# Performance work log

Hardware: AMD Instinct MI355X
Metric: run time of the kernel (lower is better)

Reference implementation:

```python
import jax, jax.numpy as jnp
import numpy as np


def _c1(x, W, b):
    # 1x1 conv: W [out,in], x [B,in,H,W]
    return jnp.einsum('oi,bihw->bohw', W, x) + b[None, :, None, None]


def _c3(x, W, b):
    # 3x3 conv, stride 1, padding 1 (SAME)
    y = jax.lax.conv_general_dilated(x, W, (1, 1), 'SAME',
                                     dimension_numbers=('NCHW', 'OIHW', 'NCHW'))
    return y + b[None, :, None, None]


def _resize(x, h, w):
    # matches torch F.interpolate(mode='bilinear', align_corners=False)
    return jax.image.resize(x, (x.shape[0], x.shape[1], h, w), 'linear', antialias=False)


def setup_inputs() -> dict:
    key = jax.random.key(0)
    ks = jax.random.split(key, 20)
    B, C, H, W = 4, 64, 128, 128
    d = C // 8

    def n(k, shape, s=0.05):
        return jax.random.normal(k, shape, dtype=jnp.float32) * s

    z = lambda c: jnp.zeros((c,), jnp.float32)
    return {
        'x': jax.random.normal(ks[0], (B, C, H, W), dtype=jnp.float32),
        'mask': jax.random.normal(ks[1], (B, 64, H, W), dtype=jnp.float32),
        'Wq': n(ks[2], (d, C)), 'bq': z(d),
        'Wk': n(ks[3], (d, C)), 'bk': z(d),
        'Wv': n(ks[4], (C, C)), 'bv': z(C),
        'alpha1': jax.random.uniform(ks[5], (1,), dtype=jnp.float32),
        'alpha2': jax.random.uniform(ks[6], (1,), dtype=jnp.float32),
        'mq_w1': n(ks[7], (64, 64, 3, 3)), 'mq_b1': z(64),
        'mq_w2': n(ks[8], (d, 64)), 'mq_b2': z(d),
        'mk_w1': n(ks[9], (64, 64, 3, 3)), 'mk_b1': z(64),
        'mk_w2': n(ks[10], (d, 64)), 'mk_b2': z(d),
        'ca_w1': n(ks[11], (64, 64)), 'ca_b1': z(64),
        'ca_w2': n(ks[12], (64, 64)), 'ca_b2': z(64),
    }


def reference(x, mask, Wq, bq, Wk, bk, Wv, bv, alpha1, alpha2,
              mq_w1, mq_b1, mq_w2, mq_b2, mk_w1, mk_b1, mk_w2, mk_b2,
              ca_w1, ca_b1, ca_w2, ca_b2):
    B, C, H, W = x.shape
    h2, w2 = H // 2, W // 2
    N = h2 * w2

    mask_q = _c1(jax.nn.relu(_c3(mask, mq_w1, mq_b1)), mq_w2, mq_b2)
    mask_k = _c1(jax.nn.relu(_c3(mask, mk_w1, mk_b1)), mk_w2, mk_b2)
    xq = _c1(x, Wq, bq)  # [B, d, H, W]
    xk = _c1(x, Wk, bk)

    pq = mask_q * xq * alpha1 + xq * (1.0 - alpha1)
    pq = _resize(pq, h2, w2).reshape(B, -1, N)          # [B, d, N]
    pk = mask_k * xk * alpha2 + xk * (1.0 - alpha2)
    pk = _resize(pk, h2, w2).reshape(B, -1, N)          # [B, d, N]

    energy = jnp.einsum('bdn,bdm->bnm', pq, pk)         # [B, N, N]
    attn = jax.nn.softmax(energy, axis=-1)

    pv = _resize(_c1(x, Wv, bv), h2, w2).reshape(B, C, N)
    out = jnp.einsum('bcn,bmn->bcm', pv, attn)          # value @ attn^T
    out = out.reshape(B, C, h2, w2)
    out = _resize(out, H, W)
    out = _c1(jax.nn.relu(_c1(out, ca_w1, ca_b1)), ca_w2, ca_b2)
    return out + x
```

## Files before the change

### kernel.cpp

```cpp
#include <hip/hip_runtime.h>
#include <hip/hip_bf16.h>

typedef _Float16 half8 __attribute__((ext_vector_type(8)));
typedef _Float16 half4v __attribute__((ext_vector_type(4)));
typedef _Float16 half2v __attribute__((ext_vector_type(2)));
typedef __fp16 pkh2 __attribute__((ext_vector_type(2)));
typedef float f32x4 __attribute__((ext_vector_type(4)));

static __device__ __forceinline__ f32x4 mfma16(half8 a, half8 b, f32x4 c) {
    return __builtin_amdgcn_mfma_f32_16x16x32_f16(a, b, c, 0, 0, 0);
}

typedef const __attribute__((address_space(1))) unsigned int* gas_ptr;
typedef __attribute__((address_space(3))) unsigned int* las_ptr;
static __device__ __forceinline__ void gload16(const void* g, void* l) {
    __builtin_amdgcn_global_load_lds((gas_ptr)g, (las_ptr)l, 16, 0, 0);
}

static __device__ __forceinline__ half2v cvt2(float a, float b) {
    pkh2 t = __builtin_amdgcn_cvt_pkrtz(a, b);
    return __builtin_bit_cast(half2v, t);
}
static __device__ __forceinline__ half8 pk8(f32x4 a, f32x4 b) {
    half2v x0 = cvt2(a[0], a[1]);
    half2v x1 = cvt2(a[2], a[3]);
    half2v x2 = cvt2(b[0], b[1]);
    half2v x3 = cvt2(b[2], b[3]);
    half4v lo = __builtin_shufflevector(x0, x1, 0, 1, 2, 3);
    half4v hi = __builtin_shufflevector(x2, x3, 0, 1, 2, 3);
    return __builtin_shufflevector(lo, hi, 0, 1, 2, 3, 4, 5, 6, 7);
}
static __device__ __forceinline__ half4v pk4(f32x4 a) {
    half2v x0 = cvt2(a[0], a[1]);
    half2v x1 = cvt2(a[2], a[3]);
    return __builtin_shufflevector(x0, x1, 0, 1, 2, 3);
}

#define WS_APCONV   0u
#define WS_APW2S    147456u
#define WS_APCA     151552u
#define WS_APW2K4   159744u
#define WS_PACKED   196608u
#define WS_MASKQ    8849408u
#define WS_MASKK    10946560u
#define WS_Q16      13043712u
#define WS_K16      13305856u
#define WS_V16      13568000u
#define WS_ZB       15665152u
#define WS_PACC8    17762304u
#define WS_PML8     34539520u
#define WS_END8     35063808u
#define WS_PACC4    WS_PACKED
#define WS_PML4     WS_MASKQ

__global__ __launch_bounds__(256) void prep_pack_kernel(
    const float* __restrict__ mask,
    const float* __restrict__ mqw1, const float* __restrict__ mkw1,
    const float* __restrict__ mqw2, const float* __restrict__ mkw2,
    const float* __restrict__ caw1, const float* __restrict__ caw2,
    _Float16* __restrict__ packed,
    _Float16* __restrict__ ApackConv, _Float16* __restrict__ ApackW2s,
    _Float16* __restrict__ ApackCA, _Float16* __restrict__ ApackW2K4)
{
    int tid = threadIdx.x;
    if (blockIdx.z < 4) {
        int ich = blockIdx.y, b = blockIdx.z;
        _Float16* Pb = packed + ((size_t)b * 8 + ich) * 130 * 130 * 8;
        if (blockIdx.x < 2) {
            for (int p = blockIdx.x * 260 + tid; p < (int)(blockIdx.x + 1) * 260; p += 256) {
                int row, col;
                if (p < 130)      { row = 0;       col = p; }
                else if (p < 260) { row = 129;     col = p - 130; }
                else if (p < 390) { row = p - 260; col = 0; }
                else              { row = p - 390; col = 129; }
                half8 z = {};
                *(half8*)(Pb + ((size_t)row * 130 + col) * 8) = z;
            }
        }
        int x = tid & 127;
        int sy = blockIdx.x * 2 + (tid >> 7);
        half8 v;
#pragma unroll
        for (int cc = 0; cc < 8; cc++)
            v[cc] = (_Float16)mask[(((size_t)(b * 64 + ich * 8 + cc)) * 128 + sy) * 128 + x];
        *(half8*)(Pb + (((size_t)(sy + 1)) * 130 + (x + 1)) * 8) = v;
        return;
    }
    int tid0 = (blockIdx.y * 64 + blockIdx.x) * 256 + tid;
    const int stride = 512 * 256;
    for (int idx = tid0; idx < 73728; idx += stride) {
        int j = idx & 7, lane = (idx >> 3) & 63, mf = (idx >> 9) & 3;
        int ks18 = idx >> 11;
        int br = ks18 / 18, kstep = ks18 % 18;
        int oc = mf * 16 + (lane & 15);
        int g = lane >> 4;
        int k = kstep * 32 + g * 8 + j;
        int tap = k >> 6, ic = k & 63;
        int dy = tap / 3, dx = tap - dy * 3;
        const float* w1 = br ? mkw1 : mqw1;
        ApackConv[idx] = (_Float16)w1[((oc * 64 + ic) * 3 + dy) * 3 + dx];
    }
    for (int idx = tid0; idx < 2048; idx += stride) {
        int j = idx & 7, lane = (idx >> 3) & 63;
        int f = (idx >> 9) & 1, br = idx >> 10;
        int dc = lane & 15, g = lane >> 4;
        int kap = 16 * (2 * f + (j >> 2)) + 4 * g + (j & 3);
        const float* w2 = br ? mkw2 : mqw2;
        ApackW2s[idx] = (_Float16)((dc < 8) ? w2[dc * 64 + kap] : 0.f);
    }
    for (int idx = tid0; idx < 4096; idx += stride) {
        int j = idx & 7, lane = (idx >> 3) & 63, mf = (idx >> 9) & 3, f = idx >> 11;
        int cp = mf * 16 + (lane & 15), g = lane >> 4;
        int kap = 16 * (2 * f + (j >> 2)) + 4 * g + (j & 3);
        ApackCA[idx] = (_Float16)caw1[cp * 64 + kap];
    }
    for (int idx = tid0; idx < 4096; idx += stride) {
        int j = idx & 7, lane = (idx >> 3) & 63, mf = (idx >> 9) & 3, f = idx >> 11;
        int cc = mf * 16 + (lane & 15), g = lane >> 4;
        int cpk = f * 32 + g * 8 + j;
        ApackW2K4[idx] = (_Float16)caw2[cc * 64 + cpk];
    }
}

__global__ __launch_bounds__(256) void conv_mask_kernel(
    const _Float16* __restrict__ packed,
    const _Float16* __restrict__ ApackConv,
    const _Float16* __restrict__ ApackW2s,
    const float* __restrict__ mqb1, const float* __restrict__ mqb2,
    const float* __restrict__ mkb1, const float* __restrict__ mkb2,
    _Float16* __restrict__ maskq, _Float16* __restrict__ maskk)
{
    __shared__ __align__(16) _Float16 A[36864];
    __shared__ __align__(16) _Float16 S[28032];
    int tid = threadIdx.x;
    int lane = tid & 63, w = tid >> 6;
    int x0 = blockIdx.x * 64;
    int y0 = blockIdx.y * 4;
    int bz = blockIdx.z;
    int b = bz >> 1, br = bz & 1;
    int q = lane & 15, g = lane >> 4;

    const _Float16* Ag = ApackConv + br * 36864;
#pragma unroll
    for (int i = 0; i < 18; i++) {
        int off = w * 9216 + i * 512;
        gload16(Ag + off + lane * 8, A + off);
    }
    const _Float16* Pb = packed + (size_t)b * 8 * 130 * 130 * 8;
#pragma unroll
    for (int i = 0; i < 12; i++) {
        int rr = w * 12 + i;
        int ich = rr / 6, pr = rr - ich * 6;
        const _Float16* src = Pb + (((size_t)ich * 130 + (y0 + pr)) * 130 + x0) * 8;
        _Float16* dst = S + (ich * 6 + pr) * 584;
        gload16(src + lane * 8, dst);
        if (lane < 8) gload16(src + (64 + lane) * 8, dst + 512);
    }
    __syncthreads();

    f32x4 acc[4][4] = {};
#pragma unroll
    for (int kstep = 0; kstep < 18; kstep++) {
        int tap = kstep >> 1;
        int dyv = tap / 3, dxv = tap - dyv * 3;
        int ich = (kstep & 1) * 4 + g;
        const _Float16* srow = S + ((ich * 6 + w + dyv) * 73 + q + dxv) * 8;
        half8 bf[4];
#pragma unroll
        for (int nf = 0; nf < 4; nf++)
            bf[nf] = *(const half8*)(srow + nf * 128);
        const _Float16* Ak = A + kstep * 2048 + lane * 8;
#pragma unroll
        for (int mf = 0; mf < 4; mf++) {
            half8 af = *(const half8*)(Ak + mf * 512);
#pragma unroll
            for (int nf = 0; nf < 4; nf++)
                acc[mf][nf] = mfma16(af, bf[nf], acc[mf][nf]);
        }
    }
    const float* b1p = br ? mkb1 : mqb1;
    const float* b2p = br ? mkb2 : mqb2;
    _Float16* outp = br ? maskk : maskq;
    float b1v[16];
#pragma unroll
    for (int mf = 0; mf < 4; mf++)
#pragma unroll
        for (int r = 0; r < 4; r++) b1v[mf * 4 + r] = b1p[mf * 16 + g * 4 + r];
    f32x4 acc2[4] = {};
#pragma unroll
    for (int f = 0; f < 2; f++) {
        half8 a2 = *(const half8*)(ApackW2s + (br * 2 + f) * 512 + lane * 8);
#pragma unroll
        for (int nf = 0; nf < 4; nf++) {
            half8 b2f;
#pragma unroll
            for (int j = 0; j < 8; j++) {
                int mfj = 2 * f + (j >> 2), rj = j & 3;
                b2f[j] = (_Float16)fmaxf(acc[mfj][nf][rj] + b1v[mfj * 4 + rj], 0.f);
            }
            acc2[nf] = mfma16(a2, b2f, acc2[nf]);
        }
    }
    if (g < 2) {
        int y = y0 + w;
#pragma unroll
        for (int r = 0; r < 4; r++) {
            int dc = g * 4 + r;
            float bb = b2p[dc];
#pragma unroll
            for (int nf = 0; nf < 4; nf++)
                outp[((size_t)(b * 8 + dc) * 128 + y) * 128 + (x0 + nf * 16 + q)] =
                    (_Float16)(acc2[nf][r] + bb);
        }
    }
}

__global__ __launch_bounds__(512) void proj_kernel(
    const float* __restrict__ xg,
    const _Float16* __restrict__ maskq, const _Float16* __restrict__ maskk,
    const float* __restrict__ Wq, const float* __restrict__ bq,
    const float* __restrict__ Wk, const float* __restrict__ bk,
    const float* __restrict__ Wv, const float* __restrict__ bv,
    const float* __restrict__ a1p, const float* __restrict__ a2p,
    _Float16* __restrict__ Qg, _Float16* __restrict__ Kg, _Float16* __restrict__ Vg)
{
    __shared__ float xr[16384];
    __shared__ float xw[4096];
    __shared__ float lWv[4096], lWq[512], lWk[512];
    int tid = threadIdx.x;
    int b = blockIdx.x >> 6, i = blockIdx.x & 63;

    for (int idx = tid; idx < 16384; idx += 512) {
        int ic = idx >> 8, rem = idx & 255;
        xr[idx] = xg[((size_t)(b * 64 + ic) * 128 + (2 * i + (rem >> 7))) * 128 + (rem & 127)];
    }
    for (int idx = tid; idx < 4096; idx += 512) lWv[idx] = Wv[idx];
    lWq[tid] = Wq[tid];
    lWk[tid] = Wk[tid];
    __syncthreads();
    for (int idx = tid; idx < 4096; idx += 512) {
        int ic = idx >> 6, j = idx & 63;
        const float* base = &xr[ic * 256 + 2 * j];
        xw[idx] = 0.25f * (base[0] + base[1] + base[128] + base[129]);
    }
    __syncthreads();

    if (tid < 256) {
        int c0 = tid >> 5;
        int j0 = (tid & 31) * 2;
        float acc0[8], acc1[8];
#pragma unroll
        for (int u = 0; u < 8; u++) { float bb = bv[c0 + 8 * u]; acc0[u] = bb; acc1[u] = bb; }
        for (int ic = 0; ic < 64; ic++) {
            float x0v = xw[ic * 64 + j0], x1v = xw[ic * 64 + j0 + 1];
#pragma unroll
            for (int u = 0; u < 8; u++) {
                float ww = lWv[(c0 + 8 * u) * 64 + ic];
                acc0[u] += ww * x0v; acc1[u] += ww * x1v;
            }
        }
        int f = j0 >> 5, gg = (j0 & 15) >> 2, hi = (j0 >> 4) & 1;
        int off = (f * 4 + gg) * 8 + (j0 & 3) + 4 * hi;
#pragma unroll
        for (int u = 0; u < 8; u++) {
            int c = c0 + 8 * u;
            _Float16* p = Vg + (size_t)(b * 64 + c) * 4096 + i * 64 + off;
            p[0] = (_Float16)acc0[u]; p[1] = (_Float16)acc1[u];
        }
    } else {
        int t = tid - 256;
        int branch = t >> 7;
        int ysel = t & 1;
        int j = (t >> 1) & 63;
        const float* W = branch ? lWk : lWq;
        const float* bias = branch ? bk : bq;
        float alpha = branch ? a2p[0] : a1p[0];
        const _Float16* mq = branch ? maskk : maskq;
        _Float16* outg = branch ? Kg : Qg;
        int x0c = 2 * j, x1c = 2 * j + 1;
        float aq0[8], aq1[8];
#pragma unroll
        for (int dc = 0; dc < 8; dc++) { float bb = bias[dc]; aq0[dc] = bb; aq1[dc] = bb; }
        for (int ic = 0; ic < 64; ic++) {
            float xv0 = xr[ic * 256 + ysel * 128 + x0c];
            float xv1 = xr[ic * 256 + ysel * 128 + x1c];
#pragma unroll
            for (int dc = 0; dc < 8; dc++) {
                float ww = W[dc * 64 + ic];
                aq0[dc] += ww * xv0; aq1[dc] += ww * xv1;
            }
        }
        int yy = 2 * i + ysel;
        half8 vq;
#pragma unroll
        for (int dc = 0; dc < 8; dc++) {
            size_t mbase = ((size_t)(b * 8 + dc) * 128 + yy) * 128;
            float m0v = (float)mq[mbase + x0c], m1v = (float)mq[mbase + x1c];
            float s = aq0[dc] * (alpha * m0v + (1.f - alpha))
                    + aq1[dc] * (alpha * m1v + (1.f - alpha));
            s += __shfl_xor(s, 1);
            vq[dc] = (_Float16)(0.25f * s);
        }
        if (ysel == 0)
            *(half8*)(outg + ((size_t)b * 4096 + i * 64 + j) * 8) = vq;
    }
}

__global__ __launch_bounds__(512, 4) void attn_kernel(
    const _Float16* __restrict__ Qg, const _Float16* __restrict__ Kg,
    const _Float16* __restrict__ Vg, const _Float16* __restrict__ ApackCA,
    _Float16* __restrict__ pacc, float* __restrict__ pml,
    int bmask, int sshift, int bbase)
{
    __shared__ __align__(16) _Float16 Vlds[8 * 4096];
    __shared__ __align__(16) _Float16 Klds[8 * 512];
    int tid = threadIdx.x, lane = tid & 63, w = tid >> 6;
    int q = lane & 15, g = lane >> 4;
    int bid = blockIdx.x;
    int qt = bid & 15, b = bbase + ((bid >> 4) & bmask), s = bid >> sshift;

    const _Float16* Kb = Kg + ((size_t)b * 4096 + s * 512) * 8;
    const _Float16* Vbase = Vg + (size_t)b * 64 * 4096 + s * 512;

    {
        gload16(Kb + (size_t)(w * 64 + lane) * 8, Klds + w * 512);
        int cc = w * 8 + (lane >> 3);
        int chl = (lane & 7) ^ (cc & 7);
        const _Float16* src0 = Vbase + (size_t)cc * 4096 + chl * 8;
#pragma unroll
        for (int t = 0; t < 8; t++)
            gload16(src0 + t * 64, Vlds + t * 4096 + w * 512);
    }
    half8 qf0 = {}, qf1 = {};
    if (g == 0) {
        int qb = qt * 256 + w * 32 + q;
        half8 r0 = *(const half8*)(Qg + ((size_t)b * 4096 + qb) * 8);
        half8 r1 = *(const half8*)(Qg + ((size_t)b * 4096 + qb + 16) * 8);
#pragma unroll
        for (int j = 0; j < 8; j++) {
            qf0[j] = (_Float16)((float)r0[j] * 1.44269504f);
            qf1[j] = (_Float16)((float)r1[j] * 1.44269504f);
        }
    }
    half8 a3[8];
#pragma unroll
    for (int i = 0; i < 8; i++) a3[i] = *(const half8*)(ApackCA + i * 512 + lane * 8);
    __syncthreads();

    half8 ones;
#pragma unroll
    for (int j = 0; j < 8; j++) ones[j] = (_Float16)1.f;

    f32x4 acc0[4] = {}, acc1[4] = {};
    f32x4 accl0 = {}, accl1 = {};
    const f32x4 zero4 = {};

#pragma unroll 2
    for (int t = 0; t < 8; t++) {
        const _Float16* Kt = Klds + t * 512;
        half8 af0 = *(const half8*)(Kt + q * 8);
        half8 af1 = *(const half8*)(Kt + (16 + q) * 8);
        half8 af2 = *(const half8*)(Kt + (32 + q) * 8);
        half8 af3 = *(const half8*)(Kt + (48 + q) * 8);

        half8 pb00, pb01, pb10, pb11;
        {
            f32x4 s0 = mfma16(af0, qf0, zero4);
            f32x4 s1 = mfma16(af1, qf0, zero4);
            f32x4 s2 = mfma16(af2, qf0, zero4);
            f32x4 s3 = mfma16(af3, qf0, zero4);
            f32x4 e0, e1, e2, e3;
#pragma unroll
            for (int r = 0; r < 4; r++) {
                e0[r] = __builtin_amdgcn_exp2f(s0[r]);
                e1[r] = __builtin_amdgcn_exp2f(s1[r]);
                e2[r] = __builtin_amdgcn_exp2f(s2[r]);
                e3[r] = __builtin_amdgcn_exp2f(s3[r]);
            }
            pb00 = pk8(e0, e1); pb01 = pk8(e2, e3);
            accl0 = mfma16(ones, pb00, accl0);
            accl0 = mfma16(ones, pb01, accl0);
        }
        {
            f32x4 s0 = mfma16(af0, qf1, zero4);
            f32x4 s1 = mfma16(af1, qf1, zero4);
            f32x4 s2 = mfma16(af2, qf1, zero4);
            f32x4 s3 = mfma16(af3, qf1, zero4);
            f32x4 e0, e1, e2, e3;
#pragma unroll
            for (int r = 0; r < 4; r++) {
                e0[r] = __builtin_amdgcn_exp2f(s0[r]);
                e1[r] = __builtin_amdgcn_exp2f(s1[r]);
                e2[r] = __builtin_amdgcn_exp2f(s2[r]);
                e3[r] = __builtin_amdgcn_exp2f(s3[r]);
            }
            pb10 = pk8(e0, e1); pb11 = pk8(e2, e3);
            accl1 = mfma16(ones, pb10, accl1);
            accl1 = mfma16(ones, pb11, accl1);
        }
        const _Float16* Vl = Vlds + t * 4096;
        int sw = q & 7;
        __builtin_amdgcn_s_setprio(1);
#pragma unroll
        for (int mfc = 0; mfc < 4; mfc++) {
            const _Float16* vr = Vl + (mfc * 16 + q) * 64;
            half8 av0 = *(const half8*)(vr + (g ^ sw) * 8);
            half8 av1 = *(const half8*)(vr + ((4 + g) ^ sw) * 8);
            acc0[mfc] = mfma16(av0, pb00, acc0[mfc]);
            acc1[mfc] = mfma16(av0, pb10, acc1[mfc]);
            acc0[mfc] = mfma16(av1, pb01, acc0[mfc]);
            acc1[mfc] = mfma16(av1, pb11, acc1[mfc]);
        }
        __builtin_amdgcn_s_setprio(0);
    }

    {
        half8 ob0 = pk8(acc0[0], acc0[1]);
        half8 ob1 = pk8(acc0[2], acc0[3]);
        f32x4 z[4] = {};
#pragma unroll
        for (int mf2 = 0; mf2 < 4; mf2++) {
            z[mf2] = mfma16(a3[mf2], ob0, z[mf2]);
            z[mf2] = mfma16(a3[4 + mf2], ob1, z[mf2]);
        }
        size_t prow = ((size_t)bid * 256 + w * 32 + q) * 64;
#pragma unroll
        for (int mf2 = 0; mf2 < 4; mf2++)
            *(half4v*)(pacc + prow + mf2 * 16 + g * 4) = pk4(z[mf2]);
        if (g == 0) pml[bid * 256 + w * 32 + q] = accl0[0];
    }
    {
        half8 ob0 = pk8(acc1[0], acc1[1]);
        half8 ob1 = pk8(acc1[2], acc1[3]);
        f32x4 z[4] = {};
#pragma unroll
        for (int mf2 = 0; mf2 < 4; mf2++) {
            z[mf2] = mfma16(a3[mf2], ob0, z[mf2]);
            z[mf2] = mfma16(a3[4 + mf2], ob1, z[mf2]);
        }
        size_t prow = ((size_t)bid * 256 + w * 32 + 16 + q) * 64;
#pragma unroll
        for (int mf2 = 0; mf2 < 4; mf2++)
            *(half4v*)(pacc + prow + mf2 * 16 + g * 4) = pk4(z[mf2]);
        if (g == 0) pml[bid * 256 + w * 32 + 16 + q] = accl1[0];
    }
}

__global__ __launch_bounds__(256) void combine_kernel(
    const _Float16* __restrict__ pacc, const float* __restrict__ pml,
    const float* __restrict__ cb1, _Float16* __restrict__ zb,
    int tps, int bbase)
{
    int T = blockIdx.x * 256 + threadIdx.x;
    int e = T & 7, row = T >> 3;
    int brel = row >> 12, qg = row & 4095;
    int qt16 = qg >> 8, ql = qg & 255;
    int tb0 = brel * 16 + qt16;

    float sum[8] = {};
    float L = 0.f;
    for (int s = 0; s < 8; s++) {
        int tile = s * tps + tb0;
        half8 v = *(const half8*)(pacc + ((size_t)tile * 256 + ql) * 64 + e * 8);
#pragma unroll
        for (int i = 0; i < 8; i++) sum[i] += (float)v[i];
        L += pml[tile * 256 + ql];
    }
    float inv = 1.f / L;
    half8 o;
#pragma unroll
    for (int i = 0; i < 8; i++) o[i] = (_Float16)(sum[i] * inv + cb1[e * 8 + i]);
    *(half8*)(zb + ((size_t)(bbase + brel) * 4096 + qg) * 64 + e * 8) = o;
}

template <int FUSED>
__global__ __launch_bounds__(512) void post_kernel(
    const _Float16* __restrict__ zg,
    const _Float16* __restrict__ pacc, const float* __restrict__ pml,
    const float* __restrict__ cb1,
    const float* __restrict__ xg,
    const _Float16* __restrict__ ApackW2K4, const float* __restrict__ cb2,
    float* __restrict__ outg)
{
    __shared__ _Float16 zt[6 * 18 * 72];
    int tid = threadIdx.x, lane = tid & 63, w = tid >> 6;
    int x0 = blockIdx.x * 32, y0 = blockIdx.y * 8, b = blockIdx.z;
    int r0 = 4 * (int)blockIdx.y - 1;
    int cbs = 16 * (int)blockIdx.x - 1;
    const _Float16* zgb = zg + (size_t)b * 4096 * 64;
    for (int idx = tid; idx < 864; idx += 512) {
        int rowi = idx >> 3, ch = idx & 7;
        int r = rowi / 18, col = rowi - r * 18;
        int zr = min(max(r0 + r, 0), 63);
        int zc = min(max(cbs + col, 0), 63);
        if constexpr (FUSED) {
            int zq = zr * 64 + zc;
            int tb = b * 16 + (zq >> 8);
            int ql = zq & 255;
            float sum[8] = {};
            float L = 0.f;
#pragma unroll
            for (int s = 0; s < 8; s++) {
                int tile = s * 64 + tb;
                half8 v = *(const half8*)(pacc + ((size_t)tile * 256 + ql) * 64 + ch * 8);
#pragma unroll
                for (int i2 = 0; i2 < 8; i2++) sum[i2] += (float)v[i2];
                L += pml[tile * 256 + ql];
            }
            float inv = 1.f / L;
            half8 o;
#pragma unroll
            for (int i2 = 0; i2 < 8; i2++) o[i2] = (_Float16)(sum[i2] * inv + cb1[ch * 8 + i2]);
            *(half8*)&zt[(r * 18 + col) * 72 + ch * 8] = o;
        } else {
            half8 v = *(const half8*)(zgb + ((size_t)(zr * 64 + zc)) * 64 + ch * 8);
            *(half8*)&zt[(r * 18 + col) * 72 + ch * 8] = v;
        }
    }
    __syncthreads();

    int q = lane & 15, g = lane >> 4;
    int y = y0 + w;
    int ra = (w >> 1) + (w & 1);
    float wyA = (w & 1) ? 0.75f : 0.25f;
    float wyB = 1.f - wyA;
    f32x4 acc[4][2] = {};
#pragma unroll
    for (int f = 0; f < 2; f++) {
        half8 a[4];
#pragma unroll
        for (int mf = 0; mf < 4; mf++)
            a[mf] = *(const half8*)(ApackW2K4 + (f * 4 + mf) * 512 + lane * 8);
#pragma unroll
        for (int nf = 0; nf < 2; nf++) {
            int pxl = nf * 16 + q;
            int ca = (pxl >> 1) + (pxl & 1);
            float wxA = (pxl & 1) ? 0.75f : 0.25f;
            float wxB = 1.f - wxA;
            half8 bfrag;
#pragma unroll
            for (int qd = 0; qd < 2; qd++) {
                int cpb = f * 32 + g * 8 + qd * 4;
                const _Float16* z00 = &zt[(ra * 18 + ca) * 72 + cpb];
                half4v h00 = *(const half4v*)z00;
                half4v h01 = *(const half4v*)(z00 + 72);
                half4v h10 = *(const half4v*)(z00 + 18 * 72);
                half4v h11 = *(const half4v*)(z00 + 18 * 72 + 72);
#pragma unroll
                for (int e = 0; e < 4; e++) {
                    float zu = ((float)h00[e] * wxA + (float)h01[e] * wxB) * wyA
                             + ((float)h10[e] * wxA + (float)h11[e] * wxB) * wyB;
                    bfrag[qd * 4 + e] = (_Float16)fmaxf(zu, 0.f);
                }
            }
#pragma unroll
            for (int mf = 0; mf < 4; mf++) acc[mf][nf] = mfma16(a[mf], bfrag, acc[mf][nf]);
        }
    }
#pragma unroll
    for (int mf = 0; mf < 4; mf++)
#pragma unroll
        for (int r = 0; r < 4; r++) {
            int c = mf * 16 + g * 4 + r;
            float bb = cb2[c];
#pragma unroll
            for (int nf = 0; nf < 2; nf++) {
                size_t oidx = ((size_t)(b * 64 + c) * 128 + y) * 128 + x0 + nf * 16 + q;
                outg[oidx] = acc[mf][nf][r] + bb + xg[oidx];
            }
        }
}

extern "C" void kernel_launch(void* const* d_in, const int* in_sizes, int n_in,
                              void* d_out, int out_size, void* d_ws, size_t ws_size,
                              hipStream_t stream)
{
    const float* x    = (const float*)d_in[0];
    const float* mask = (const float*)d_in[1];
    const float* Wq   = (const float*)d_in[2];
    const float* bq   = (const float*)d_in[3];
    const float* Wk   = (const float*)d_in[4];
    const float* bk   = (const float*)d_in[5];
    const float* Wv   = (const float*)d_in[6];
    const float* bv   = (const float*)d_in[7];
    const float* a1   = (const float*)d_in[8];
    const float* a2   = (const float*)d_in[9];
    const float* mqw1 = (const float*)d_in[10];
    const float* mqb1 = (const float*)d_in[11];
    const float* mqw2 = (const float*)d_in[12];
    const float* mqb2 = (const float*)d_in[13];
    const float* mkw1 = (const float*)d_in[14];
    const float* mkb1 = (const float*)d_in[15];
    const float* mkw2 = (const float*)d_in[16];
    const float* mkb2 = (const float*)d_in[17];
    const float* caw1 = (const float*)d_in[18];
    const float* cab1 = (const float*)d_in[19];
    const float* caw2 = (const float*)d_in[20];
    const float* cab2 = (const float*)d_in[21];

    char* ws = (char*)d_ws;
    _Float16* ApackConv = (_Float16*)(ws + WS_APCONV);
    _Float16* ApackW2s  = (_Float16*)(ws + WS_APW2S);
    _Float16* ApackCA   = (_Float16*)(ws + WS_APCA);
    _Float16* ApackW2K4 = (_Float16*)(ws + WS_APW2K4);
    _Float16* packed    = (_Float16*)(ws + WS_PACKED);
    _Float16* maskq     = (_Float16*)(ws + WS_MASKQ);
    _Float16* maskk     = (_Float16*)(ws + WS_MASKK);
    _Float16* Qg16      = (_Float16*)(ws + WS_Q16);
    _Float16* Kg16      = (_Float16*)(ws + WS_K16);
    _Float16* Vb        = (_Float16*)(ws + WS_V16);
    _Float16* zb        = (_Float16*)(ws + WS_ZB);

    prep_pack_kernel<<<dim3(64, 8, 5), dim3(256), 0, stream>>>(
        mask, mqw1, mkw1, mqw2, mkw2, caw1, caw2,
        packed, ApackConv, ApackW2s, ApackCA, ApackW2K4);
    conv_mask_kernel<<<dim3(2, 32, 8), dim3(256), 0, stream>>>(
        packed, ApackConv, ApackW2s, mqb1, mqb2, mkb1, mkb2, maskq, maskk);
    proj_kernel<<<dim3(256), dim3(512), 0, stream>>>(
        x, maskq, maskk, Wq, bq, Wk, bk, Wv, bv, a1, a2, Qg16, Kg16, Vb);

    bool big = (ws_size >= (size_t)WS_END8);
    if (big) {
        _Float16* pacc = (_Float16*)(ws + WS_PACC8);
        float*    pml  = (float*)(ws + WS_PML8);
        attn_kernel<<<dim3(512), dim3(512), 0, stream>>>(
            Qg16, Kg16, Vb, ApackCA, pacc, pml, 3, 6, 0);
        post_kernel<1><<<dim3(4, 16, 4), dim3(512), 0, stream>>>(
            zb, pacc, pml, cab1, x, ApackW2K4, cab2, (float*)d_out);
    } else {
        _Float16* pacc = (_Float16*)(ws + WS_PACC4);
        float*    pml  = (float*)(ws + WS_PML4);
        for (int bbase = 0; bbase < 4; bbase += 2) {
            attn_kernel<<<dim3(256), dim3(512), 0, stream>>>(
                Qg16, Kg16, Vb, ApackCA, pacc, pml, 1, 5, bbase);
            combine_kernel<<<dim3(256), dim3(256), 0, stream>>>(pacc, pml, cab1, zb, 32, bbase);
        }
        post_kernel<0><<<dim3(4, 16, 4), dim3(512), 0, stream>>>(
            zb, nullptr, nullptr, cab1, x, ApackW2K4, cab2, (float*)d_out);
    }
}
```

Baseline: 65.56 us.

## Fold mask packing and weight repacking into consumer kernels, drop prep kernel

Removes the separate prep kernel that converted the mask to padded fp16 and pre-packed weights into MFMA fragment layout. The conv kernel now reads fp32 mask directly with boundary handling into shared memory and packs conv weights itself. The attention and post kernels build their weight fragments from fp32 weights in registers. This saves one launch and a global round trip of the packed mask, but every block now repeats the weight packing and does scattered fp32 loads and scalar LDS stores.

```diff
diff --git a/kernel.cpp b/kernel.cpp
--- a/kernel.cpp
+++ b/kernel.cpp
@@ -36,11 +36,6 @@
     return __builtin_shufflevector(x0, x1, 0, 1, 2, 3);
 }
 
-#define WS_APCONV   0u
-#define WS_APW2S    147456u
-#define WS_APCA     151552u
-#define WS_APW2K4   159744u
-#define WS_PACKED   196608u
 #define WS_MASKQ    8849408u
 #define WS_MASKK    10946560u
 #define WS_Q16      13043712u
@@ -50,82 +45,13 @@
 #define WS_PACC8    17762304u
 #define WS_PML8     34539520u
 #define WS_END8     35063808u
-#define WS_PACC4    WS_PACKED
-#define WS_PML4     WS_MASKQ
-
-__global__ __launch_bounds__(256) void prep_pack_kernel(
+#define WS_PACC4    196608u
+#define WS_PML4     8585216u
+
+__global__ __launch_bounds__(256) void conv_mask_kernel(
     const float* __restrict__ mask,
     const float* __restrict__ mqw1, const float* __restrict__ mkw1,
     const float* __restrict__ mqw2, const float* __restrict__ mkw2,
-    const float* __restrict__ caw1, const float* __restrict__ caw2,
-    _Float16* __restrict__ packed,
-    _Float16* __restrict__ ApackConv, _Float16* __restrict__ ApackW2s,
-    _Float16* __restrict__ ApackCA, _Float16* __restrict__ ApackW2K4)
-{
-    int tid = threadIdx.x;
-    if (blockIdx.z < 4) {
-        int ich = blockIdx.y, b = blockIdx.z;
-        _Float16* Pb = packed + ((size_t)b * 8 + ich) * 130 * 130 * 8;
-        if (blockIdx.x < 2) {
-            for (int p = blockIdx.x * 260 + tid; p < (int)(blockIdx.x + 1) * 260; p += 256) {
-                int row, col;
-                if (p < 130)      { row = 0;       col = p; }
-                else if (p < 260) { row = 129;     col = p - 130; }
-                else if (p < 390) { row = p - 260; col = 0; }
-                else              { row = p - 390; col = 129; }
-                half8 z = {};
-                *(half8*)(Pb + ((size_t)row * 130 + col) * 8) = z;
-            }
-        }
-        int x = tid & 127;
-        int sy = blockIdx.x * 2 + (tid >> 7);
-        half8 v;
-#pragma unroll
-        for (int cc = 0; cc < 8; cc++)
-            v[cc] = (_Float16)mask[(((size_t)(b * 64 + ich * 8 + cc)) * 128 + sy) * 128 + x];
-        *(half8*)(Pb + (((size_t)(sy + 1)) * 130 + (x + 1)) * 8) = v;
-        return;
-    }
-    int tid0 = (blockIdx.y * 64 + blockIdx.x) * 256 + tid;
-    const int stride = 512 * 256;
-    for (int idx = tid0; idx < 73728; idx += stride) {
-        int j = idx & 7, lane = (idx >> 3) & 63, mf = (idx >> 9) & 3;
-        int ks18 = idx >> 11;
-        int br = ks18 / 18, kstep = ks18 % 18;
-        int oc = mf * 16 + (lane & 15);
-        int g = lane >> 4;
-        int k = kstep * 32 + g * 8 + j;
-        int tap = k >> 6, ic = k & 63;
-        int dy = tap / 3, dx = tap - dy * 3;
-        const float* w1 = br ? mkw1 : mqw1;
-        ApackConv[idx] = (_Float16)w1[((oc * 64 + ic) * 3 + dy) * 3 + dx];
-    }
-    for (int idx = tid0; idx < 2048; idx += stride) {
-        int j = idx & 7, lane = (idx >> 3) & 63;
-        int f = (idx >> 9) & 1, br = idx >> 10;
-        int dc = lane & 15, g = lane >> 4;
-        int kap = 16 * (2 * f + (j >> 2)) + 4 * g + (j & 3);
-        const float* w2 = br ? mkw2 : mqw2;
-        ApackW2s[idx] = (_Float16)((dc < 8) ? w2[dc * 64 + kap] : 0.f);
-    }
-    for (int idx = tid0; idx < 4096; idx += stride) {
-        int j = idx & 7, lane = (idx >> 3) & 63, mf = (idx >> 9) & 3, f = idx >> 11;
-        int cp = mf * 16 + (lane & 15), g = lane >> 4;
-        int kap = 16 * (2 * f + (j >> 2)) + 4 * g + (j & 3);
-        ApackCA[idx] = (_Float16)caw1[cp * 64 + kap];
-    }
-    for (int idx = tid0; idx < 4096; idx += stride) {
-        int j = idx & 7, lane = (idx >> 3) & 63, mf = (idx >> 9) & 3, f = idx >> 11;
-        int cc = mf * 16 + (lane & 15), g = lane >> 4;
-        int cpk = f * 32 + g * 8 + j;
-        ApackW2K4[idx] = (_Float16)caw2[cc * 64 + cpk];
-    }
-}
-
-__global__ __launch_bounds__(256) void conv_mask_kernel(
-    const _Float16* __restrict__ packed,
-    const _Float16* __restrict__ ApackConv,
-    const _Float16* __restrict__ ApackW2s,
     const float* __restrict__ mqb1, const float* __restrict__ mqb2,
     const float* __restrict__ mkb1, const float* __restrict__ mkb2,
     _Float16* __restrict__ maskq, _Float16* __restrict__ maskk)
@@ -140,21 +66,41 @@
     int b = bz >> 1, br = bz & 1;
     int q = lane & 15, g = lane >> 4;
 
-    const _Float16* Ag = ApackConv + br * 36864;
-#pragma unroll
-    for (int i = 0; i < 18; i++) {
-        int off = w * 9216 + i * 512;
-        gload16(Ag + off + lane * 8, A + off);
-    }
-    const _Float16* Pb = packed + (size_t)b * 8 * 130 * 130 * 8;
-#pragma unroll
-    for (int i = 0; i < 12; i++) {
-        int rr = w * 12 + i;
-        int ich = rr / 6, pr = rr - ich * 6;
-        const _Float16* src = Pb + (((size_t)ich * 130 + (y0 + pr)) * 130 + x0) * 8;
-        _Float16* dst = S + (ich * 6 + pr) * 584;
-        gload16(src + lane * 8, dst);
-        if (lane < 8) gload16(src + (64 + lane) * 8, dst + 512);
+    const float* w1 = br ? mkw1 : mqw1;
+    for (int idx = tid; idx < 36864; idx += 256) {
+        int j = idx & 7, ln = (idx >> 3) & 63, mf = (idx >> 9) & 3;
+        int kstep = idx >> 11;
+        int oc = mf * 16 + (ln & 15);
+        int g2 = ln >> 4;
+        int k = kstep * 32 + g2 * 8 + j;
+        int tap = k >> 6, ic = k & 63;
+        int dy = tap / 3, dx = tap - dy * 3;
+        A[idx] = (_Float16)w1[((oc * 64 + ic) * 3 + dy) * 3 + dx];
+    }
+    for (int idx = tid; idx < 6528; idx += 256) {
+        int u = idx % 17;
+        int cr = idx / 17;
+        int r = cr % 6, c = cr / 6;
+        int y = y0 - 1 + r;
+        int xb = x0 - 1 + 4 * u;
+        f32x4 v = {};
+        if (y >= 0 && y < 128) {
+            const float* mrow = mask + ((size_t)(b * 64 + c) * 128 + y) * 128;
+            if (xb >= 0 && xb <= 124) {
+                v = *(const f32x4*)(mrow + xb);
+            } else {
+#pragma unroll
+                for (int e = 0; e < 4; e++) {
+                    int xx = xb + e;
+                    if (xx >= 0 && xx < 128) v[e] = mrow[xx];
+                }
+            }
+        }
+        _Float16* dst = S + (((c >> 3) * 6 + r) * 73) * 8 + (c & 7);
+        int col0 = 4 * u;
+#pragma unroll
+        for (int e = 0; e < 4; e++)
+            dst[(col0 + e) * 8] = (_Float16)v[e];
     }
     __syncthreads();
 
@@ -180,16 +126,27 @@
     }
     const float* b1p = br ? mkb1 : mqb1;
     const float* b2p = br ? mkb2 : mqb2;
+    const float* w2 = br ? mkw2 : mqw2;
     _Float16* outp = br ? maskk : maskq;
     float b1v[16];
 #pragma unroll
     for (int mf = 0; mf < 4; mf++)
 #pragma unroll
         for (int r = 0; r < 4; r++) b1v[mf * 4 + r] = b1p[mf * 16 + g * 4 + r];
+    half8 a2f[2];
+    {
+        int dc = lane & 15;
+#pragma unroll
+        for (int f = 0; f < 2; f++)
+#pragma unroll
+            for (int j = 0; j < 8; j++) {
+                int kap = 16 * (2 * f + (j >> 2)) + 4 * (lane >> 4) + (j & 3);
+                a2f[f][j] = (_Float16)((dc < 8) ? w2[dc * 64 + kap] : 0.f);
+            }
+    }
     f32x4 acc2[4] = {};
 #pragma unroll
     for (int f = 0; f < 2; f++) {
-        half8 a2 = *(const half8*)(ApackW2s + (br * 2 + f) * 512 + lane * 8);
 #pragma unroll
         for (int nf = 0; nf < 4; nf++) {
             half8 b2f;
@@ -198,7 +155,7 @@
                 int mfj = 2 * f + (j >> 2), rj = j & 3;
                 b2f[j] = (_Float16)fmaxf(acc[mfj][nf][rj] + b1v[mfj * 4 + rj], 0.f);
             }
-            acc2[nf] = mfma16(a2, b2f, acc2[nf]);
+            acc2[nf] = mfma16(a2f[f], b2f, acc2[nf]);
         }
     }
     if (g < 2) {
@@ -235,8 +192,8 @@
         xr[idx] = xg[((size_t)(b * 64 + ic) * 128 + (2 * i + (rem >> 7))) * 128 + (rem & 127)];
     }
     for (int idx = tid; idx < 4096; idx += 512) lWv[idx] = Wv[idx];
-    lWq[tid] = Wq[tid];
-    lWk[tid] = Wk[tid];
+    lWq[tid & 511] = Wq[tid & 511];
+    lWk[tid & 511] = Wk[tid & 511];
     __syncthreads();
     for (int idx = tid; idx < 4096; idx += 512) {
         int ic = idx >> 6, j = idx & 63;
@@ -308,7 +265,7 @@
 
 __global__ __launch_bounds__(512, 4) void attn_kernel(
     const _Float16* __restrict__ Qg, const _Float16* __restrict__ Kg,
-    const _Float16* __restrict__ Vg, const _Float16* __restrict__ ApackCA,
+    const _Float16* __restrict__ Vg, const float* __restrict__ caw1,
     _Float16* __restrict__ pacc, float* __restrict__ pml,
     int bmask, int sshift, int bbase)
 {
@@ -344,7 +301,14 @@
     }
     half8 a3[8];
 #pragma unroll
-    for (int i = 0; i < 8; i++) a3[i] = *(const half8*)(ApackCA + i * 512 + lane * 8);
+    for (int i = 0; i < 8; i++) {
+        int cp = (i & 3) * 16 + (lane & 15);
+#pragma unroll
+        for (int j = 0; j < 8; j++) {
+            int kap = 16 * (2 * (i >> 2) + (j >> 2)) + 4 * (lane >> 4) + (j & 3);
+            a3[i][j] = (_Float16)caw1[cp * 64 + kap];
+        }
+    }
     __syncthreads();
 
     half8 ones;
@@ -479,7 +443,7 @@
     const _Float16* __restrict__ pacc, const float* __restrict__ pml,
     const float* __restrict__ cb1,
     const float* __restrict__ xg,
-    const _Float16* __restrict__ ApackW2K4, const float* __restrict__ cb2,
+    const float* __restrict__ caw2, const float* __restrict__ cb2,
     float* __restrict__ outg)
 {
     __shared__ _Float16 zt[6 * 18 * 72];
@@ -517,6 +481,16 @@
             *(half8*)&zt[(r * 18 + col) * 72 + ch * 8] = v;
         }
     }
+    half8 aW[8];
+#pragma unroll
+    for (int i = 0; i < 8; i++) {
+        int cc = (i & 3) * 16 + (lane & 15);
+#pragma unroll
+        for (int j = 0; j < 8; j++) {
+            int cpk = (i >> 2) * 32 + (lane >> 4) * 8 + j;
+            aW[i][j] = (_Float16)caw2[cc * 64 + cpk];
+        }
+    }
     __syncthreads();
 
     int q = lane & 15, g = lane >> 4;
@@ -527,10 +501,6 @@
     f32x4 acc[4][2] = {};
 #pragma unroll
     for (int f = 0; f < 2; f++) {
-        half8 a[4];
-#pragma unroll
-        for (int mf = 0; mf < 4; mf++)
-            a[mf] = *(const half8*)(ApackW2K4 + (f * 4 + mf) * 512 + lane * 8);
 #pragma unroll
         for (int nf = 0; nf < 2; nf++) {
             int pxl = nf * 16 + q;
@@ -554,7 +524,7 @@
                 }
             }
 #pragma unroll
-            for (int mf = 0; mf < 4; mf++) acc[mf][nf] = mfma16(a[mf], bfrag, acc[mf][nf]);
+            for (int mf = 0; mf < 4; mf++) acc[mf][nf] = mfma16(aW[f * 4 + mf], bfrag, acc[mf][nf]);
         }
     }
 #pragma unroll
@@ -599,23 +569,15 @@
     const float* cab2 = (const float*)d_in[21];
 
     char* ws = (char*)d_ws;
-    _Float16* ApackConv = (_Float16*)(ws + WS_APCONV);
-    _Float16* ApackW2s  = (_Float16*)(ws + WS_APW2S);
-    _Float16* ApackCA   = (_Float16*)(ws + WS_APCA);
-    _Float16* ApackW2K4 = (_Float16*)(ws + WS_APW2K4);
-    _Float16* packed    = (_Float16*)(ws + WS_PACKED);
-    _Float16* maskq     = (_Float16*)(ws + WS_MASKQ);
-    _Float16* maskk     = (_Float16*)(ws + WS_MASKK);
-    _Float16* Qg16      = (_Float16*)(ws + WS_Q16);
-    _Float16* Kg16      = (_Float16*)(ws + WS_K16);
-    _Float16* Vb        = (_Float16*)(ws + WS_V16);
-    _Float16* zb        = (_Float16*)(ws + WS_ZB);
-
-    prep_pack_kernel<<<dim3(64, 8, 5), dim3(256), 0, stream>>>(
-        mask, mqw1, mkw1, mqw2, mkw2, caw1, caw2,
-        packed, ApackConv, ApackW2s, ApackCA, ApackW2K4);
+    _Float16* maskq = (_Float16*)(ws + WS_MASKQ);
+    _Float16* maskk = (_Float16*)(ws + WS_MASKK);
+    _Float16* Qg16  = (_Float16*)(ws + WS_Q16);
+    _Float16* Kg16  = (_Float16*)(ws + WS_K16);
+    _Float16* Vb    = (_Float16*)(ws + WS_V16);
+    _Float16* zb    = (_Float16*)(ws + WS_ZB);
+
     conv_mask_kernel<<<dim3(2, 32, 8), dim3(256), 0, stream>>>(
-        packed, ApackConv, ApackW2s, mqb1, mqb2, mkb1, mkb2, maskq, maskk);
+        mask, mqw1, mkw1, mqw2, mkw2, mqb1, mqb2, mkb1, mkb2, maskq, maskk);
     proj_kernel<<<dim3(256), dim3(512), 0, stream>>>(
         x, maskq, maskk, Wq, bq, Wk, bk, Wv, bv, a1, a2, Qg16, Kg16, Vb);
 
@@ -624,18 +586,18 @@
         _Float16* pacc = (_Float16*)(ws + WS_PACC8);
         float*    pml  = (float*)(ws + WS_PML8);
         attn_kernel<<<dim3(512), dim3(512), 0, stream>>>(
-            Qg16, Kg16, Vb, ApackCA, pacc, pml, 3, 6, 0);
+            Qg16, Kg16, Vb, caw1, pacc, pml, 3, 6, 0);
         post_kernel<1><<<dim3(4, 16, 4), dim3(512), 0, stream>>>(
-            zb, pacc, pml, cab1, x, ApackW2K4, cab2, (float*)d_out);
+            zb, pacc, pml, cab1, x, caw2, cab2, (float*)d_out);
     } else {
         _Float16* pacc = (_Float16*)(ws + WS_PACC4);
         float*    pml  = (float*)(ws + WS_PML4);
         for (int bbase = 0; bbase < 4; bbase += 2) {
             attn_kernel<<<dim3(256), dim3(512), 0, stream>>>(
-                Qg16, Kg16, Vb, ApackCA, pacc, pml, 1, 5, bbase);
+                Qg16, Kg16, Vb, caw1, pacc, pml, 1, 5, bbase);
             combine_kernel<<<dim3(256), dim3(256), 0, stream>>>(pacc, pml, cab1, zb, 32, bbase);
         }
         post_kernel<0><<<dim3(4, 16, 4), dim3(512), 0, stream>>>(
-            zb, nullptr, nullptr, cab1, x, ApackW2K4, cab2, (float*)d_out);
-    }
-}
+            zb, nullptr, nullptr, cab1, x, caw2, cab2, (float*)d_out);
+    }
+}
```

After: 136.0 us. 2.07x slower.
